# Kernel optimization log

Measured on AMD Instinct MI355X. Metric: run time of the kernel, lower is better.

## Reference

```python
import jax, jax.numpy as jnp
import numpy as np

N, E, B = 20000, 60000, 512
F_IN, ED, H, C = 7, 3, 4, 256
HC = H * C  # 1024
D_MODEL = 1024
EPS_BN = 1e-5


def setup_inputs() -> dict:
    key = jax.random.key(0)
    ks = jax.random.split(key, 24)
    s = 0.05
    inp = {
        'x': jax.random.normal(ks[0], (N, F_IN), jnp.float32),
        'edge_index': jax.random.randint(ks[1], (2, E), 0, N, jnp.int32),
        'edge_attr': jax.random.normal(ks[2], (E, ED), jnp.float32),
        'batch': jnp.sort(jax.random.randint(ks[3], (N,), 0, B, jnp.int32)),
        'w0': jax.random.normal(ks[4], (F_IN, HC), jnp.float32) * s,
        'w_rest': jax.random.normal(ks[5], (3, HC, HC), jnp.float32) * s,
        'w_edge': jax.random.normal(ks[6], (4, ED, HC), jnp.float32) * s,
        'att_src': jax.random.normal(ks[7], (4, H, C), jnp.float32) * s,
        'att_dst': jax.random.normal(ks[8], (4, H, C), jnp.float32) * s,
        'att_edge': jax.random.normal(ks[9], (4, H, C), jnp.float32) * s,
        'bias012': jax.random.normal(ks[10], (3, HC), jnp.float32) * s,
        'bias3': jax.random.normal(ks[11], (C,), jnp.float32) * s,
        'bn_gamma': jnp.ones((3, HC), jnp.float32),
        'bn_beta': jnp.zeros((3, HC), jnp.float32),
        'bn_mean': jnp.zeros((3, HC), jnp.float32),
        'bn_var': jnp.ones((3, HC), jnp.float32),
        'gate_w': jax.random.normal(ks[12], (C, 1), jnp.float32) * s,
        'gate_b': jnp.zeros((1,), jnp.float32),
        'proj_w': jax.random.normal(ks[13], (C, D_MODEL), jnp.float32) * s,
        'proj_b': jnp.zeros((D_MODEL,), jnp.float32),
    }
    return inp


def _gat_layer(x, ei, ea, W, We, a_s, a_d, a_e, bias, concat):
    # PyG GATConv with edge_dim, add_self_loops=True (fill_value='mean'), eval mode (no dropout)
    n = x.shape[0]
    sl = jnp.arange(n, dtype=ei.dtype)
    ea_mean = ea.mean(axis=0)
    ei = jnp.concatenate([ei, jnp.stack([sl, sl])], axis=1)            # [2, E+N]
    ea = jnp.concatenate([ea, jnp.broadcast_to(ea_mean, (n, ea.shape[1]))], axis=0)
    h = (x @ W).reshape(n, H, C)                                       # [N,H,C]
    alpha_src = jnp.einsum('nhc,hc->nh', h, a_s)
    alpha_dst = jnp.einsum('nhc,hc->nh', h, a_d)
    eh = (ea @ We).reshape(-1, H, C)
    alpha_e = jnp.einsum('ehc,hc->eh', eh, a_e)
    src, dst = ei[0], ei[1]
    alpha = jax.nn.leaky_relu(alpha_src[src] + alpha_dst[dst] + alpha_e, 0.2)  # [E+N,H]
    amax = jax.ops.segment_max(alpha, dst, num_segments=n)
    alpha = jnp.exp(alpha - amax[dst])
    denom = jax.ops.segment_sum(alpha, dst, num_segments=n)
    alpha = alpha / (denom[dst] + 1e-16)
    msg = h[src] * alpha[:, :, None]                                   # [E+N,H,C]
    out = jax.ops.segment_sum(msg, dst, num_segments=n)                # [N,H,C]
    out = out.reshape(n, H * C) if concat else out.mean(axis=1)
    return out + bias


def reference(x, edge_index, edge_attr, batch, w0, w_rest, w_edge, att_src, att_dst,
              att_edge, bias012, bias3, bn_gamma, bn_beta, bn_mean, bn_var,
              gate_w, gate_b, proj_w, proj_b):
    h = x
    for i in range(4):
        W = w0 if i == 0 else w_rest[i - 1]
        concat = i < 3
        b = bias012[i] if concat else bias3
        h = _gat_layer(h, edge_index, edge_attr, W, w_edge[i],
                       att_src[i], att_dst[i], att_edge[i], b, concat)
        if i < 3:
            # BatchNorm1d in eval mode, then ReLU (dropout is identity in eval)
            h = (h - bn_mean[i]) * (bn_gamma[i] / jnp.sqrt(bn_var[i] + EPS_BN)) + bn_beta[i]
            h = jax.nn.relu(h)
    # AttentionalAggregation: segment softmax over gate scores, weighted sum per graph
    gate = h @ gate_w + gate_b                                         # [N,1]
    gmax = jax.ops.segment_max(gate, batch, num_segments=B)
    g = jnp.exp(gate - gmax[batch])
    gsum = jax.ops.segment_sum(g, batch, num_segments=B)
    w = g / (gsum[batch] + 1e-16)
    graph = jax.ops.segment_sum(w * h, batch, num_segments=B)          # [B,256]
    return graph @ proj_w + proj_b                                     # [B,1024]
```

## Files before the change

### kernel.cpp

```cpp
#include <hip/hip_runtime.h>
#include <math.h>

#define NN 20000
#define NP 20480
#define EE 60000
#define BB 512
#define HC 1024
#define HH 4
#define CC 256

typedef _Float16 f16;
typedef f16 half8 __attribute__((ext_vector_type(8)));
typedef f16 f16x4 __attribute__((ext_vector_type(4)));
typedef float floatx4 __attribute__((ext_vector_type(4)));
typedef float floatx16 __attribute__((ext_vector_type(16)));

__device__ __forceinline__ size_t af_off(int n, int c) {
    int mblk = n >> 7, rr = n & 127;
    int iter = c >> 5, kc = c & 31;
    int kh = kc >> 4, kg = (kc >> 3) & 1, e = kc & 7;
    return ((((size_t)(mblk * 32 + iter) * 2 + kh) * 4 + (rr >> 5)) * 64 +
            (kg * 32 + (rr & 31))) * 8 + e;
}

__global__ void ea_sum_kernel(const float* __restrict__ ea, float* sums, int E_) {
    float s0 = 0.f, s1 = 0.f, s2 = 0.f;
    for (int e = blockIdx.x * 256 + threadIdx.x; e < E_; e += gridDim.x * 256) {
        s0 += ea[e * 3 + 0];
        s1 += ea[e * 3 + 1];
        s2 += ea[e * 3 + 2];
    }
    for (int o = 32; o; o >>= 1) {
        s0 += __shfl_down(s0, o);
        s1 += __shfl_down(s1, o);
        s2 += __shfl_down(s2, o);
    }
    if ((threadIdx.x & 63) == 0) {
        atomicAdd(&sums[0], s0);
        atomicAdd(&sums[1], s1);
        atomicAdd(&sums[2], s2);
    }
}

__global__ void hist_kernel(const int* __restrict__ ei, int* counts, int E_) {
    int e = blockIdx.x * 256 + threadIdx.x;
    if (e < E_) atomicAdd(&counts[ei[E_ + e]], 1);
}

__global__ void scan1_kernel(const int* __restrict__ counts, int* __restrict__ partial,
                             int* __restrict__ psums, int n) {
    __shared__ int sdata[256];
    int t = threadIdx.x;
    int i = blockIdx.x * 256 + t;
    int v = (i < n) ? counts[i] : 0;
    sdata[t] = v;
    __syncthreads();
#pragma unroll
    for (int off = 1; off < 256; off <<= 1) {
        int tmp = (t >= off) ? sdata[t - off] : 0;
        __syncthreads();
        sdata[t] += tmp;
        __syncthreads();
    }
    if (i < n) partial[i] = sdata[t];
    if (t == 255) psums[blockIdx.x] = sdata[255];
}

__global__ void scan2_kernel(int* __restrict__ psums, int nb) {
    __shared__ int sdata[128];
    int t = threadIdx.x;
    sdata[t] = (t < nb) ? psums[t] : 0;
    __syncthreads();
#pragma unroll
    for (int off = 1; off < 128; off <<= 1) {
        int tmp = (t >= off) ? sdata[t - off] : 0;
        __syncthreads();
        sdata[t] += tmp;
        __syncthreads();
    }
    if (t < nb) psums[t] = (t == 0) ? 0 : sdata[t - 1];
}

__global__ void scan3_kernel(const int* __restrict__ partial, const int* __restrict__ psums,
                             int* __restrict__ indptr, int n) {
    int i = blockIdx.x * 256 + threadIdx.x;
    if (i == 0) indptr[0] = 0;
    if (i < n) indptr[i + 1] = partial[i] + psums[blockIdx.x];
}

__global__ void scatter_kernel(const int* __restrict__ ei, const int* __restrict__ indptr,
                               int* fill, int* sorted, int* sdst, int E_) {
    int e = blockIdx.x * 256 + threadIdx.x;
    if (e >= E_) return;
    int d = ei[E_ + e];
    int pos = indptr[d] + atomicAdd(&fill[d], 1);
    sorted[pos] = e;
    sdst[pos] = d;
}

__global__ void bptr_kernel(const int* __restrict__ batch, int* bptr, int n, int nb) {
    int i = blockIdx.x * 256 + threadIdx.x;
    if (i >= n) return;
    int b = batch[i];
    if (i == 0) {
        for (int bb = 0; bb <= b; bb++) bptr[bb] = 0;
    } else {
        int pb = batch[i - 1];
        if (pb != b) {
            for (int bb = pb + 1; bb <= b; bb++) bptr[bb] = i;
        }
    }
    if (i == n - 1) {
        for (int bb = b + 1; bb <= nb; bb++) bptr[bb] = n;
    }
}

__global__ void wconv_kernel(const float* __restrict__ w_rest, f16* __restrict__ wt) {
    __shared__ float tile[64][65];
    int l = blockIdx.z;
    int bx = blockIdx.x * 64;
    int by = blockIdx.y * 64;
    int t = threadIdx.x;
    int tr = t >> 6, tc = t & 63;
#pragma unroll
    for (int i = 0; i < 16; i++) {
        int r = by + i * 4 + tr;
        tile[i * 4 + tr][tc] = w_rest[(size_t)l * 1048576 + (size_t)r * 1024 + bx + tc];
    }
    __syncthreads();
#pragma unroll
    for (int i = 0; i < 16; i++) {
        int n = bx + i * 4 + tr;
        wt[(size_t)l * 1048576 + (size_t)n * 1024 + by + tc] = (f16)tile[tc][i * 4 + tr];
    }
}

__global__ void bfrs_kernel(const f16* __restrict__ wt, f16* __restrict__ Bf) {
    int iter = blockIdx.x, nblk = blockIdx.y, l = blockIdx.z;
    const f16* wl = wt + (size_t)l * 1048576;
    f16* bl = Bf + (size_t)l * 1048576;
    int t = threadIdx.x;
    for (int c = t; c < 512; c += 256) {
        int kh = c >> 8, rem = c & 255, cg = rem >> 6, lane = rem & 63;
        int n = nblk * 128 + cg * 32 + (lane & 31);
        int k = iter * 32 + (kh * 2 + (lane >> 5)) * 8;
        half8 v = *(const half8*)&wl[(size_t)n * 1024 + k];
        *(half8*)&bl[(size_t)(nblk * 32 + iter) * 4096 + c * 8] = v;
    }
}

__global__ void mmat_all_kernel(const float* __restrict__ w_edge,
                                const float* __restrict__ att_edge,
                                const float* __restrict__ ea_sums, float* Mmat,
                                float* ae_self, float invE) {
    __shared__ float red[256];
    __shared__ float Ms[12];
    int l = blockIdx.x;
    int t = threadIdx.x;
    for (int dh = 0; dh < 12; dh++) {
        int d = dh >> 2, hh = dh & 3;
        float v = w_edge[l * 3072 + d * HC + hh * CC + t] * att_edge[l * HC + hh * CC + t];
        red[t] = v;
        __syncthreads();
        for (int o = 128; o; o >>= 1) {
            if (t < o) red[t] += red[t + o];
            __syncthreads();
        }
        if (t == 0) {
            Ms[dh] = red[0];
            Mmat[l * 12 + dh] = red[0];
        }
        __syncthreads();
    }
    if (t < 4) {
        float v = 0.f;
        for (int d = 0; d < 3; d++) v += ea_sums[d] * invE * Ms[d * 4 + t];
        ae_self[l * 4 + t] = v;
    }
}

__global__ void pack_kernel(const int* __restrict__ ei, const int* __restrict__ sorted,
                            const float* __restrict__ ea, const float* __restrict__ Mmat,
                            int* __restrict__ ssrc, float* __restrict__ aeh_pk) {
    int idx = blockIdx.x * 256 + threadIdx.x;
    if (idx >= EE) return;
    int eid = sorted[idx];
    ssrc[idx] = ei[eid];
    float a0 = ea[eid * 3 + 0], a1 = ea[eid * 3 + 1], a2 = ea[eid * 3 + 2];
#pragma unroll
    for (int l = 0; l < 4; l++) {
#pragma unroll
        for (int h = 0; h < 4; h++) {
            aeh_pk[(size_t)idx * 16 + l * 4 + h] =
                a0 * Mmat[l * 12 + h] + a1 * Mmat[l * 12 + 4 + h] + a2 * Mmat[l * 12 + 8 + h];
        }
    }
}

__global__ void edgep_kernel(const int* __restrict__ ssrc, const int* __restrict__ sdst,
                             const float* __restrict__ aeh_pk, const float* __restrict__ asrc,
                             const float* __restrict__ adst, float* __restrict__ pe,
                             int layer) {
    int i = blockIdx.x * 256 + threadIdx.x;
    if (i >= EE) return;
    int src = ssrc[i];
    int dst = sdst[i];
    float4 a = *(const float4*)&asrc[(size_t)src * 4];
    float4 d = *(const float4*)&adst[(size_t)dst * 4];
    float4 m = *(const float4*)&aeh_pk[(size_t)i * 16 + layer * 4];
    float r[4] = {a.x + d.x + m.x, a.y + d.y + m.y, a.z + d.z + m.z, a.w + d.w + m.w};
    float4 o;
#pragma unroll
    for (int k = 0; k < 4; k++) {
        float v = (r[k] > 0.f) ? r[k] : 0.2f * r[k];
        (&o.x)[k] = __expf(v);
    }
    *(float4*)&pe[(size_t)i * 4] = o;
}

__global__ void bnss_kernel(const float* __restrict__ bias012, const float* __restrict__ bn_g,
                            const float* __restrict__ bn_b, const float* __restrict__ bn_m,
                            const float* __restrict__ bn_v, float2* __restrict__ bnss) {
    int i = blockIdx.x * 256 + threadIdx.x;
    if (i >= 3 * HC) return;
    float s = bn_g[i] * rsqrtf(bn_v[i] + 1e-5f);
    float2 o;
    o.x = s;
    o.y = (bias012[i] - bn_m[i]) * s + bn_b[i];
    bnss[i] = o;
}

__global__ void wvec_kernel(const float* __restrict__ w_rest, const float* __restrict__ att_src,
                            const float* __restrict__ att_dst, float* __restrict__ wsv,
                            float* __restrict__ wdv) {
    int l = blockIdx.y;
    int k = blockIdx.x;
    int t = threadIdx.x;
    int hp = t >> 6, lane = t & 63;
    int col = hp * 256 + lane * 4;
    const float* wrow = w_rest + (size_t)l * 1048576 + (size_t)k * 1024;
    float4 w4 = *(const float4*)&wrow[col];
    float4 a4 = *(const float4*)&att_src[(l + 1) * HC + col];
    float4 d4 = *(const float4*)&att_dst[(l + 1) * HC + col];
    float sp = w4.x * a4.x + w4.y * a4.y + w4.z * a4.z + w4.w * a4.w;
    float dp = w4.x * d4.x + w4.y * d4.y + w4.z * d4.z + w4.w * d4.w;
    for (int m = 1; m < 64; m <<= 1) {
        sp += __shfl_xor(sp, m);
        dp += __shfl_xor(dp, m);
    }
    if (lane == 0) {
        wsv[((size_t)l * 1024 + k) * 4 + hp] = sp;
        wdv[((size_t)l * 1024 + k) * 4 + hp] = dp;
    }
}

__global__ void w0vec_kernel(const float* __restrict__ w0, const float* __restrict__ att_src,
                             const float* __restrict__ att_dst, float* __restrict__ w0s,
                             float* __restrict__ w0d) {
    int f = blockIdx.x;
    int t = threadIdx.x;
    int hp = t >> 6, lane = t & 63;
    int col = hp * 256 + lane * 4;
    float4 w4 = *(const float4*)&w0[f * HC + col];
    float4 a4 = *(const float4*)&att_src[col];
    float4 d4 = *(const float4*)&att_dst[col];
    float sp = w4.x * a4.x + w4.y * a4.y + w4.z * a4.z + w4.w * a4.w;
    float dp = w4.x * d4.x + w4.y * d4.y + w4.z * d4.z + w4.w * d4.w;
    for (int m = 1; m < 64; m <<= 1) {
        sp += __shfl_xor(sp, m);
        dp += __shfl_xor(dp, m);
    }
    if (lane == 0) {
        w0s[f * 4 + hp] = sp;
        w0d[f * 4 + hp] = dp;
    }
}

__global__ void alpha0_kernel(const float* __restrict__ x, const float* __restrict__ w0s,
                              const float* __restrict__ w0d, float* __restrict__ asrc,
                              float* __restrict__ adst) {
    int n = blockIdx.x * 256 + threadIdx.x;
    if (n >= NN) return;
    float xr[7];
#pragma unroll
    for (int f = 0; f < 7; f++) xr[f] = x[n * 7 + f];
#pragma unroll
    for (int hp = 0; hp < 4; hp++) {
        float s = 0.f, d = 0.f;
#pragma unroll
        for (int f = 0; f < 7; f++) {
            s += xr[f] * w0s[f * 4 + hp];
            d += xr[f] * w0d[f * 4 + hp];
        }
        asrc[n * 4 + hp] = s;
        adst[n * 4 + hp] = d;
    }
}

__global__ void agg0x_kernel(const float* __restrict__ x, const float* __restrict__ asrc,
                             const float* __restrict__ adst, const float* __restrict__ ae_self,
                             const int* __restrict__ ssrc, const float* __restrict__ pe,
                             const int* __restrict__ indptr, float* __restrict__ xagg) {
    int n = blockIdx.x * 256 + threadIdx.x;
    if (n >= NN) return;
    float4 as4 = *(const float4*)&asrc[(size_t)n * 4];
    float4 ad4 = *(const float4*)&adst[(size_t)n * 4];
    float adl[4] = {ad4.x, ad4.y, ad4.z, ad4.w};
    float asl[4] = {as4.x, as4.y, as4.z, as4.w};
    float xr[7];
#pragma unroll
    for (int f = 0; f < 7; f++) xr[f] = x[n * 7 + f];
    float denom[4];
    float xa[4][7];
#pragma unroll
    for (int h = 0; h < 4; h++) {
        float r = asl[h] + adl[h] + ae_self[h];
        r = (r > 0.f) ? r : 0.2f * r;
        float p = __expf(r);
        denom[h] = p;
#pragma unroll
        for (int f = 0; f < 7; f++) xa[h][f] = p * xr[f];
    }
    int s = indptr[n], e = indptr[n + 1];
    for (int idx = s; idx < e; idx++) {
        int src = ssrc[idx];
        float4 pv = *(const float4*)&pe[(size_t)idx * 4];
        float pl[4] = {pv.x, pv.y, pv.z, pv.w};
        float xs[7];
#pragma unroll
        for (int f = 0; f < 7; f++) xs[f] = x[src * 7 + f];
#pragma unroll
        for (int h = 0; h < 4; h++) {
            denom[h] += pl[h];
#pragma unroll
            for (int f = 0; f < 7; f++) xa[h][f] += pl[h] * xs[f];
        }
    }
#pragma unroll
    for (int h = 0; h < 4; h++) {
        float inv = 1.0f / (denom[h] + 1e-16f);
#pragma unroll
        for (int f = 0; f < 7; f++) xagg[(size_t)n * 28 + h * 7 + f] = xa[h][f] * inv;
    }
}

__global__ void gemm7f_kernel(const float* __restrict__ xagg, const float* __restrict__ w0,
                              const float2* __restrict__ bnss, const float* __restrict__ wsv,
                              const float* __restrict__ wdv, f16* __restrict__ outAf,
                              float* __restrict__ asrc_n, float* __restrict__ adst_n) {
    __shared__ float xs[28];
    __shared__ float red[32];
    int n = blockIdx.x, t = threadIdx.x;
    if (t < 28) xs[t] = xagg[(size_t)n * 28 + t];
    __syncthreads();
    int head = t >> 6;
    int j0 = t * 4;
    float sp[4] = {0.f, 0.f, 0.f, 0.f}, dp[4] = {0.f, 0.f, 0.f, 0.f};
    f16x4 o;
#pragma unroll
    for (int k = 0; k < 4; k++) {
        int j = j0 + k;
        float dot = 0.f;
#pragma unroll
        for (int f = 0; f < 7; f++) dot += xs[head * 7 + f] * w0[f * HC + j];
        float2 ss = bnss[j];
        float val = fmaxf(fmaf(dot, ss.x, ss.y), 0.f);
        o[k] = (f16)val;
        float4 w4s = *(const float4*)&wsv[(size_t)j * 4];
        float4 w4d = *(const float4*)&wdv[(size_t)j * 4];
        sp[0] += val * w4s.x; sp[1] += val * w4s.y;
        sp[2] += val * w4s.z; sp[3] += val * w4s.w;
        dp[0] += val * w4d.x; dp[1] += val * w4d.y;
        dp[2] += val * w4d.z; dp[3] += val * w4d.w;
    }
    *(f16x4*)&outAf[af_off(n, j0)] = o;
    int wave = t >> 6, lane = t & 63;
#pragma unroll
    for (int m = 1; m < 64; m <<= 1) {
#pragma unroll
        for (int j = 0; j < 4; j++) {
            sp[j] += __shfl_xor(sp[j], m);
            dp[j] += __shfl_xor(dp[j], m);
        }
    }
    if (lane == 0) {
#pragma unroll
        for (int j = 0; j < 4; j++) {
            red[wave * 8 + j] = sp[j];
            red[wave * 8 + 4 + j] = dp[j];
        }
    }
    __syncthreads();
    if (t < 8) {
        float v = red[t] + red[8 + t] + red[16 + t] + red[24 + t];
        if (t < 4) asrc_n[n * 4 + t] = v;
        else adst_n[n * 4 + (t - 4)] = v;
    }
}

__global__ __launch_bounds__(256) void mfma_gemm_kernel(const f16* __restrict__ Af,
                                                        const f16* __restrict__ Bf,
                                                        f16* __restrict__ C16) {
    int t = threadIdx.x;
    int wave = t >> 6, lane = t & 63;
    int gid = blockIdx.x;
    int g = gid >> 6, rblk = gid & 63;
    int nblk = rblk >> 3;
    int mblk = g * 8 + (rblk & 7);
    int rg0 = (wave >> 1) * 2;
    int cg0 = (wave & 1) * 2;

    floatx16 acc[2][2];
#pragma unroll
    for (int i = 0; i < 2; i++)
#pragma unroll
        for (int j = 0; j < 2; j++) acc[i][j] = (floatx16)(0.f);

    const f16* pa = Af + (size_t)mblk * 131072 + (size_t)lane * 8;
    const f16* pb = Bf + (size_t)nblk * 131072 + (size_t)lane * 8;

#pragma unroll 2
    for (int iter = 0; iter < 32; iter++) {
        size_t base = (size_t)iter * 4096;
        half8 afr[2][2], bfr[2][2];
#pragma unroll
        for (int kh = 0; kh < 2; kh++) {
#pragma unroll
            for (int i = 0; i < 2; i++) {
                afr[kh][i] = *(const half8*)&pa[base + kh * 2048 + (rg0 + i) * 512];
                bfr[kh][i] = *(const half8*)&pb[base + kh * 2048 + (cg0 + i) * 512];
            }
        }
#pragma unroll
        for (int kh = 0; kh < 2; kh++)
#pragma unroll
            for (int i = 0; i < 2; i++)
#pragma unroll
                for (int j = 0; j < 2; j++)
                    acc[i][j] = __builtin_amdgcn_mfma_f32_32x32x16_f16(bfr[kh][j], afr[kh][i],
                                                                       acc[i][j], 0, 0, 0);
    }

    int fr32 = lane & 31, kg = lane >> 5;
#pragma unroll
    for (int i = 0; i < 2; i++) {
        int row = mblk * 128 + rg0 * 32 + i * 32 + fr32;
#pragma unroll
        for (int j = 0; j < 2; j++) {
#pragma unroll
            for (int gq = 0; gq < 4; gq++) {
                f16x4 o;
#pragma unroll
                for (int r = 0; r < 4; r++) o[r] = (f16)acc[i][j][gq * 4 + r];
                *(f16x4*)&C16[(size_t)row * HC + nblk * 128 + cg0 * 32 + j * 32 + gq * 8 +
                              kg * 4] = o;
            }
        }
    }
}

__global__ void agg_kernel(const f16* __restrict__ h16, const float* __restrict__ asrc,
                           const float* __restrict__ adst, const float* __restrict__ ae_self,
                           const int* __restrict__ ssrc, const float* __restrict__ pe,
                           const int* __restrict__ indptr, const float2* __restrict__ bnss,
                           const float* __restrict__ wsv, const float* __restrict__ wdv,
                           const float* __restrict__ bias3, const float* __restrict__ gw,
                           const float* __restrict__ gb, f16* __restrict__ out16,
                           float* __restrict__ asrc_n, float* __restrict__ adst_n,
                           float* __restrict__ out3, float* __restrict__ gate,
                           int layer, int concat) {
    __shared__ float buf[1024];
    __shared__ float red[32];
    int n = blockIdx.x, t = threadIdx.x;
    int h = t >> 6, lane = t & 63;
    int c4 = t * 4;

    float r = asrc[n * 4 + h] + adst[n * 4 + h] + ae_self[layer * 4 + h];
    r = (r > 0.f) ? r : 0.2f * r;
    float p = __expf(r);
    float denom = p;
    float ax, ay, az, aw;
    {
        f16x4 v = *(const f16x4*)&h16[(size_t)n * HC + c4];
        ax = p * (float)v[0]; ay = p * (float)v[1];
        az = p * (float)v[2]; aw = p * (float)v[3];
    }
    int s = indptr[n], epos = indptr[n + 1];
    for (int base = s; base < epos; base += 4) {
        int rem = epos - base;
        int src[4];
        float pv[4];
#pragma unroll
        for (int j = 0; j < 4; j++) {
            if (j < rem) {
                src[j] = ssrc[base + j];
                pv[j] = pe[(size_t)(base + j) * 4 + h];
            } else {
                src[j] = n;
                pv[j] = 0.f;
            }
        }
        f16x4 u[4];
#pragma unroll
        for (int j = 0; j < 4; j++) u[j] = *(const f16x4*)&h16[(size_t)src[j] * HC + c4];
#pragma unroll
        for (int j = 0; j < 4; j++) {
            denom += pv[j];
            ax += pv[j] * (float)u[j][0];
            ay += pv[j] * (float)u[j][1];
            az += pv[j] * (float)u[j][2];
            aw += pv[j] * (float)u[j][3];
        }
    }
    float inv = 1.0f / (denom + 1e-16f);
    ax *= inv; ay *= inv; az *= inv; aw *= inv;

    if (concat) {
        float vals[4] = {ax, ay, az, aw};
        f16x4 o;
        float sp[4] = {0.f, 0.f, 0.f, 0.f}, dp[4] = {0.f, 0.f, 0.f, 0.f};
#pragma unroll
        for (int k = 0; k < 4; k++) {
            int j = c4 + k;
            float2 ss = bnss[j];
            float val = fmaxf(fmaf(vals[k], ss.x, ss.y), 0.f);
            o[k] = (f16)val;
            float4 w4s = *(const float4*)&wsv[(size_t)j * 4];
            float4 w4d = *(const float4*)&wdv[(size_t)j * 4];
            sp[0] += val * w4s.x; sp[1] += val * w4s.y;
            sp[2] += val * w4s.z; sp[3] += val * w4s.w;
            dp[0] += val * w4d.x; dp[1] += val * w4d.y;
            dp[2] += val * w4d.z; dp[3] += val * w4d.w;
        }
        *(f16x4*)&out16[af_off(n, c4)] = o;
#pragma unroll
        for (int m = 1; m < 64; m <<= 1) {
#pragma unroll
            for (int j = 0; j < 4; j++) {
                sp[j] += __shfl_xor(sp[j], m);
                dp[j] += __shfl_xor(dp[j], m);
            }
        }
        if (lane == 0) {
#pragma unroll
            for (int j = 0; j < 4; j++) {
                red[h * 8 + j] = sp[j];
                red[h * 8 + 4 + j] = dp[j];
            }
        }
        __syncthreads();
        if (t < 8) {
            float v = red[t] + red[8 + t] + red[16 + t] + red[24 + t];
            if (t < 4) asrc_n[n * 4 + t] = v;
            else adst_n[n * 4 + (t - 4)] = v;
        }
    } else {
        buf[c4 + 0] = ax;
        buf[c4 + 1] = ay;
        buf[c4 + 2] = az;
        buf[c4 + 3] = aw;
        __syncthreads();
        if (t < 64) {
            float gpart = 0.f;
#pragma unroll
            for (int k = 0; k < 4; k++) {
                int c = t * 4 + k;
                float v2 = 0.25f * (buf[c] + buf[256 + c] + buf[512 + c] + buf[768 + c]) +
                           bias3[c];
                out3[(size_t)n * CC + c] = v2;
                gpart += v2 * gw[c];
            }
            for (int o = 32; o; o >>= 1) gpart += __shfl_down(gpart, o);
            if (t == 0) gate[n] = gpart + gb[0];
        }
    }
}

__global__ void graphagg_kernel(const float* __restrict__ gate, const float* __restrict__ h3,
                                const int* __restrict__ bptr, float* __restrict__ graph) {
    __shared__ float red[256];
    __shared__ float wn[256];
    int b = blockIdx.x, t = threadIdx.x;
    int s = bptr[b], epos = bptr[b + 1];
    float m = -3.4e38f;
    for (int n = s + t; n < epos; n += 256) m = fmaxf(m, gate[n]);
    red[t] = m;
    __syncthreads();
    for (int o = 128; o; o >>= 1) {
        if (t < o) red[t] = fmaxf(red[t], red[t + o]);
        __syncthreads();
    }
    float mval = red[0];
    __syncthreads();
    float sum = 0.f;
    for (int n = s + t; n < epos; n += 256) sum += __expf(gate[n] - mval);
    red[t] = sum;
    __syncthreads();
    for (int o = 128; o; o >>= 1) {
        if (t < o) red[t] += red[t + o];
        __syncthreads();
    }
    float ssum = red[0];
    __syncthreads();
    float acc = 0.f;
    for (int base = s; base < epos; base += 256) {
        int n = base + t;
        wn[t] = (n < epos) ? __expf(gate[n] - mval) : 0.f;
        __syncthreads();
        int cnt = min(256, epos - base);
        for (int j = 0; j < cnt; j++) acc += wn[j] * h3[(size_t)(base + j) * CC + t];
        __syncthreads();
    }
    graph[b * CC + t] = acc / (ssum + 1e-16f);
}

__global__ void proj_kernel(const float* __restrict__ graph, const float* __restrict__ pw,
                            const float* __restrict__ pb, float* __restrict__ out) {
    __shared__ float g[256];
    int b = blockIdx.x, t = threadIdx.x;
    g[t] = graph[b * CC + t];
    __syncthreads();
    for (int j = t; j < 1024; j += 256) {
        float acc = pb[j];
        for (int c = 0; c < 256; c++) acc += g[c] * pw[c * 1024 + j];
        out[(size_t)b * 1024 + j] = acc;
    }
}

extern "C" void kernel_launch(void* const* d_in, const int* in_sizes, int n_in,
                              void* d_out, int out_size, void* d_ws, size_t ws_size,
                              hipStream_t stream) {
    const float* x = (const float*)d_in[0];
    const int* ei = (const int*)d_in[1];
    const float* ea = (const float*)d_in[2];
    const int* batch = (const int*)d_in[3];
    const float* w0 = (const float*)d_in[4];
    const float* w_rest = (const float*)d_in[5];
    const float* w_edge = (const float*)d_in[6];
    const float* att_src = (const float*)d_in[7];
    const float* att_dst = (const float*)d_in[8];
    const float* att_edge = (const float*)d_in[9];
    const float* bias012 = (const float*)d_in[10];
    const float* bias3 = (const float*)d_in[11];
    const float* bn_g = (const float*)d_in[12];
    const float* bn_b = (const float*)d_in[13];
    const float* bn_m = (const float*)d_in[14];
    const float* bn_v = (const float*)d_in[15];
    const float* gate_w = (const float*)d_in[16];
    const float* gate_b = (const float*)d_in[17];
    const float* proj_w = (const float*)d_in[18];
    const float* proj_b = (const float*)d_in[19];
    float* out = (float*)d_out;

    float* ws = (float*)d_ws;
    size_t off = 0;
    f16* h_lin = (f16*)(ws + off); off += (size_t)NP * HC / 2;
    f16* h_af = (f16*)(ws + off); off += (size_t)NP * HC / 2;
    float* h3 = ws + off; off += (size_t)NN * CC;
    f16* wt = (f16*)(ws + off); off += (size_t)3 * HC * HC / 2;
    f16* Bf = (f16*)(ws + off); off += (size_t)3 * HC * HC / 2;
    float* asrcA = ws + off; off += (size_t)NN * 4;
    float* adstA = ws + off; off += (size_t)NN * 4;
    float* asrcB = ws + off; off += (size_t)NN * 4;
    float* adstB = ws + off; off += (size_t)NN * 4;
    float* wsv = ws + off; off += (size_t)3 * HC * 4;
    float* wdv = ws + off; off += (size_t)3 * HC * 4;
    float* w0s = ws + off; off += 28;
    float* w0d = ws + off; off += 28;
    float2* bnss = (float2*)(ws + off); off += (size_t)3 * HC * 2;
    float* aeh_pk = ws + off; off += (size_t)EE * 16;
    float* pbuf = ws + off; off += (size_t)EE * 4;
    float* xagg = ws + off; off += (size_t)NN * 28;
    float* gate = ws + off; off += (size_t)NN;
    float* graph = ws + off; off += (size_t)BB * CC;
    float* ea_sums = ws + off; off += 4;
    float* Mmat = ws + off; off += 48;
    float* ae_self = ws + off; off += 16;
    int* counts = (int*)(ws + off); off += NN;
    int* partial = (int*)(ws + off); off += NN;
    int* psums = (int*)(ws + off); off += 128;
    int* indptr = (int*)(ws + off); off += NN + 1;
    int* fill = (int*)(ws + off); off += NN;
    int* sorted = (int*)(ws + off); off += EE;
    int* ssrc = (int*)(ws + off); off += EE;
    int* sdst = (int*)(ws + off); off += EE;
    int* bptr = (int*)(ws + off); off += BB + 1;

    hipMemsetAsync(ea_sums, 0, 4 * sizeof(float), stream);
    hipMemsetAsync(counts, 0, NN * sizeof(int), stream);
    hipMemsetAsync(fill, 0, NN * sizeof(int), stream);

    ea_sum_kernel<<<64, 256, 0, stream>>>(ea, ea_sums, EE);
    hist_kernel<<<(EE + 255) / 256, 256, 0, stream>>>(ei, counts, EE);
    int nblk = (NN + 255) / 256;
    scan1_kernel<<<nblk, 256, 0, stream>>>(counts, partial, psums, NN);
    scan2_kernel<<<1, 128, 0, stream>>>(psums, nblk);
    scan3_kernel<<<nblk, 256, 0, stream>>>(partial, psums, indptr, NN);
    scatter_kernel<<<(EE + 255) / 256, 256, 0, stream>>>(ei, indptr, fill, sorted, sdst, EE);
    bptr_kernel<<<(NN + 255) / 256, 256, 0, stream>>>(batch, bptr, NN, BB);
    wconv_kernel<<<dim3(16, 16, 3), 256, 0, stream>>>(w_rest, wt);
    bfrs_kernel<<<dim3(32, 8, 3), 256, 0, stream>>>(wt, Bf);
    mmat_all_kernel<<<4, 256, 0, stream>>>(w_edge, att_edge, ea_sums, Mmat, ae_self,
                                           1.0f / EE);
    pack_kernel<<<(EE + 255) / 256, 256, 0, stream>>>(ei, sorted, ea, Mmat, ssrc, aeh_pk);
    bnss_kernel<<<(3 * HC + 255) / 256, 256, 0, stream>>>(bias012, bn_g, bn_b, bn_m, bn_v,
                                                          bnss);
    wvec_kernel<<<dim3(1024, 3), 256, 0, stream>>>(w_rest, att_src, att_dst, wsv, wdv);
    w0vec_kernel<<<7, 256, 0, stream>>>(w0, att_src, att_dst, w0s, w0d);
    alpha0_kernel<<<(NN + 255) / 256, 256, 0, stream>>>(x, w0s, w0d, asrcA, adstA);

    edgep_kernel<<<(EE + 255) / 256, 256, 0, stream>>>(ssrc, sdst, aeh_pk, asrcA, adstA,
                                                       pbuf, 0);
    agg0x_kernel<<<(NN + 255) / 256, 256, 0, stream>>>(x, asrcA, adstA, ae_self, ssrc,
                                                       pbuf, indptr, xagg);
    gemm7f_kernel<<<NN, 256, 0, stream>>>(xagg, w0, bnss, wsv, wdv, h_af, asrcB, adstB);

    float* asrc_cur = asrcB;
    float* adst_cur = adstB;
    float* asrc_nxt = asrcA;
    float* adst_nxt = adstA;
    for (int i = 1; i < 4; i++) {
        mfma_gemm_kernel<<<(NP / 128) * (HC / 128), 256, 0, stream>>>(
            h_af, Bf + (size_t)(i - 1) * HC * HC, h_lin);
        edgep_kernel<<<(EE + 255) / 256, 256, 0, stream>>>(ssrc, sdst, aeh_pk, asrc_cur,
                                                           adst_cur, pbuf, i);
        agg_kernel<<<NN, 256, 0, stream>>>(
            h_lin, asrc_cur, adst_cur, ae_self, ssrc, pbuf, indptr, bnss + (size_t)i * HC,
            wsv + (size_t)i * HC * 4, wdv + (size_t)i * HC * 4, bias3, gate_w, gate_b,
            h_af, asrc_nxt, adst_nxt, h3, gate, i, (i < 3) ? 1 : 0);
        float* tmp = asrc_cur; asrc_cur = asrc_nxt; asrc_nxt = tmp;
        tmp = adst_cur; adst_cur = adst_nxt; adst_nxt = tmp;
    }

    graphagg_kernel<<<BB, 256, 0, stream>>>(gate, h3, bptr, graph);
    proj_kernel<<<BB, 256, 0, stream>>>(graph, proj_w, proj_b, out);
}
```

Before: 680.6 us.

## Map one node per wavefront in aggregation and layer-0 GEMM kernels

The agg and gemm7f kernels move from one 256-thread block per node to one 64-lane wavefront per node, with each lane handling 16 contiguous channels through 16-byte half8 loads. Cross-head reductions now use wave shuffles instead of shared memory and __syncthreads, and the final-layer head averaging uses xor shuffles across the 16-lane groups. This removes block-level synchronization and shared-memory traffic and widens the neighbor gather loads. In exchange it uses more registers per lane and has fewer waves in flight per node, which may lower occupancy and the memory parallelism available to the gathers.

```diff
diff --git a/kernel.cpp b/kernel.cpp
--- a/kernel.cpp
+++ b/kernel.cpp
@@ -348,24 +348,41 @@
                               const float2* __restrict__ bnss, const float* __restrict__ wsv,
                               const float* __restrict__ wdv, f16* __restrict__ outAf,
                               float* __restrict__ asrc_n, float* __restrict__ adst_n) {
-    __shared__ float xs[28];
-    __shared__ float red[32];
-    int n = blockIdx.x, t = threadIdx.x;
-    if (t < 28) xs[t] = xagg[(size_t)n * 28 + t];
-    __syncthreads();
-    int head = t >> 6;
-    int j0 = t * 4;
+    int t = threadIdx.x;
+    int wv = t >> 6, lane = t & 63;
+    int n = blockIdx.x * 4 + wv;
+    int h = lane >> 4;
+    int cb = lane << 4;
+
+    float xv = (lane < 28) ? xagg[(size_t)n * 28 + lane] : 0.f;
+    float xs[7];
+#pragma unroll
+    for (int f = 0; f < 7; f++) xs[f] = __shfl(xv, h * 7 + f);
+
+    float dot[16];
+#pragma unroll
+    for (int k = 0; k < 16; k++) dot[k] = 0.f;
+#pragma unroll
+    for (int f = 0; f < 7; f++) {
+        const float* wrow = w0 + (size_t)f * HC + cb;
+#pragma unroll
+        for (int k = 0; k < 16; k += 4) {
+            float4 w4 = *(const float4*)&wrow[k];
+            dot[k + 0] += xs[f] * w4.x;
+            dot[k + 1] += xs[f] * w4.y;
+            dot[k + 2] += xs[f] * w4.z;
+            dot[k + 3] += xs[f] * w4.w;
+        }
+    }
+
     float sp[4] = {0.f, 0.f, 0.f, 0.f}, dp[4] = {0.f, 0.f, 0.f, 0.f};
-    f16x4 o;
-#pragma unroll
-    for (int k = 0; k < 4; k++) {
-        int j = j0 + k;
-        float dot = 0.f;
-#pragma unroll
-        for (int f = 0; f < 7; f++) dot += xs[head * 7 + f] * w0[f * HC + j];
+    half8 o0, o1;
+#pragma unroll
+    for (int k = 0; k < 8; k++) {
+        int j = cb + k;
         float2 ss = bnss[j];
-        float val = fmaxf(fmaf(dot, ss.x, ss.y), 0.f);
-        o[k] = (f16)val;
+        float val = fmaxf(fmaf(dot[k], ss.x, ss.y), 0.f);
+        o0[k] = (f16)val;
         float4 w4s = *(const float4*)&wsv[(size_t)j * 4];
         float4 w4d = *(const float4*)&wdv[(size_t)j * 4];
         sp[0] += val * w4s.x; sp[1] += val * w4s.y;
@@ -373,8 +390,21 @@
         dp[0] += val * w4d.x; dp[1] += val * w4d.y;
         dp[2] += val * w4d.z; dp[3] += val * w4d.w;
     }
-    *(f16x4*)&outAf[af_off(n, j0)] = o;
-    int wave = t >> 6, lane = t & 63;
+#pragma unroll
+    for (int k = 0; k < 8; k++) {
+        int j = cb + 8 + k;
+        float2 ss = bnss[j];
+        float val = fmaxf(fmaf(dot[8 + k], ss.x, ss.y), 0.f);
+        o1[k] = (f16)val;
+        float4 w4s = *(const float4*)&wsv[(size_t)j * 4];
+        float4 w4d = *(const float4*)&wdv[(size_t)j * 4];
+        sp[0] += val * w4s.x; sp[1] += val * w4s.y;
+        sp[2] += val * w4s.z; sp[3] += val * w4s.w;
+        dp[0] += val * w4d.x; dp[1] += val * w4d.y;
+        dp[2] += val * w4d.z; dp[3] += val * w4d.w;
+    }
+    *(half8*)&outAf[af_off(n, cb)] = o0;
+    *(half8*)&outAf[af_off(n, cb + 8)] = o1;
 #pragma unroll
     for (int m = 1; m < 64; m <<= 1) {
 #pragma unroll
@@ -384,17 +414,11 @@
         }
     }
     if (lane == 0) {
-#pragma unroll
-        for (int j = 0; j < 4; j++) {
-            red[wave * 8 + j] = sp[j];
-            red[wave * 8 + 4 + j] = dp[j];
-        }
-    }
-    __syncthreads();
-    if (t < 8) {
-        float v = red[t] + red[8 + t] + red[16 + t] + red[24 + t];
-        if (t < 4) asrc_n[n * 4 + t] = v;
-        else adst_n[n * 4 + (t - 4)] = v;
+        float4 so, ddo;
+        so.x = sp[0]; so.y = sp[1]; so.z = sp[2]; so.w = sp[3];
+        ddo.x = dp[0]; ddo.y = dp[1]; ddo.z = dp[2]; ddo.w = dp[3];
+        *(float4*)&asrc_n[(size_t)n * 4] = so;
+        *(float4*)&adst_n[(size_t)n * 4] = ddo;
     }
 }
 
@@ -469,21 +493,25 @@
                            float* __restrict__ asrc_n, float* __restrict__ adst_n,
                            float* __restrict__ out3, float* __restrict__ gate,
                            int layer, int concat) {
-    __shared__ float buf[1024];
-    __shared__ float red[32];
-    int n = blockIdx.x, t = threadIdx.x;
-    int h = t >> 6, lane = t & 63;
-    int c4 = t * 4;
+    int t = threadIdx.x;
+    int wv = t >> 6, lane = t & 63;
+    int n = blockIdx.x * 4 + wv;
+    int h = lane >> 4;
+    int cb = lane << 4;
 
     float r = asrc[n * 4 + h] + adst[n * 4 + h] + ae_self[layer * 4 + h];
     r = (r > 0.f) ? r : 0.2f * r;
     float p = __expf(r);
     float denom = p;
-    float ax, ay, az, aw;
+    float acc[16];
     {
-        f16x4 v = *(const f16x4*)&h16[(size_t)n * HC + c4];
-        ax = p * (float)v[0]; ay = p * (float)v[1];
-        az = p * (float)v[2]; aw = p * (float)v[3];
+        half8 v0 = *(const half8*)&h16[(size_t)n * HC + cb];
+        half8 v1 = *(const half8*)&h16[(size_t)n * HC + cb + 8];
+#pragma unroll
+        for (int k = 0; k < 8; k++) {
+            acc[k] = p * (float)v0[k];
+            acc[8 + k] = p * (float)v1[k];
+        }
     }
     int s = indptr[n], epos = indptr[n + 1];
     for (int base = s; base < epos; base += 4) {
@@ -500,31 +528,35 @@
                 pv[j] = 0.f;
             }
         }
-        f16x4 u[4];
-#pragma unroll
-        for (int j = 0; j < 4; j++) u[j] = *(const f16x4*)&h16[(size_t)src[j] * HC + c4];
+        half8 u0[4], u1[4];
+#pragma unroll
+        for (int j = 0; j < 4; j++) {
+            u0[j] = *(const half8*)&h16[(size_t)src[j] * HC + cb];
+            u1[j] = *(const half8*)&h16[(size_t)src[j] * HC + cb + 8];
+        }
 #pragma unroll
         for (int j = 0; j < 4; j++) {
             denom += pv[j];
-            ax += pv[j] * (float)u[j][0];
-            ay += pv[j] * (float)u[j][1];
-            az += pv[j] * (float)u[j][2];
-            aw += pv[j] * (float)u[j][3];
+#pragma unroll
+            for (int k = 0; k < 8; k++) {
+                acc[k] += pv[j] * (float)u0[j][k];
+                acc[8 + k] += pv[j] * (float)u1[j][k];
+            }
         }
     }
     float inv = 1.0f / (denom + 1e-16f);
-    ax *= inv; ay *= inv; az *= inv; aw *= inv;
+#pragma unroll
+    for (int k = 0; k < 16; k++) acc[k] *= inv;
 
     if (concat) {
-        float vals[4] = {ax, ay, az, aw};
-        f16x4 o;
         float sp[4] = {0.f, 0.f, 0.f, 0.f}, dp[4] = {0.f, 0.f, 0.f, 0.f};
-#pragma unroll
-        for (int k = 0; k < 4; k++) {
-            int j = c4 + k;
+        half8 o0, o1;
+#pragma unroll
+        for (int k = 0; k < 8; k++) {
+            int j = cb + k;
             float2 ss = bnss[j];
-            float val = fmaxf(fmaf(vals[k], ss.x, ss.y), 0.f);
-            o[k] = (f16)val;
+            float val = fmaxf(fmaf(acc[k], ss.x, ss.y), 0.f);
+            o0[k] = (f16)val;
             float4 w4s = *(const float4*)&wsv[(size_t)j * 4];
             float4 w4d = *(const float4*)&wdv[(size_t)j * 4];
             sp[0] += val * w4s.x; sp[1] += val * w4s.y;
@@ -532,7 +564,21 @@
             dp[0] += val * w4d.x; dp[1] += val * w4d.y;
             dp[2] += val * w4d.z; dp[3] += val * w4d.w;
         }
-        *(f16x4*)&out16[af_off(n, c4)] = o;
+#pragma unroll
+        for (int k = 0; k < 8; k++) {
+            int j = cb + 8 + k;
+            float2 ss = bnss[j];
+            float val = fmaxf(fmaf(acc[8 + k], ss.x, ss.y), 0.f);
+            o1[k] = (f16)val;
+            float4 w4s = *(const float4*)&wsv[(size_t)j * 4];
+            float4 w4d = *(const float4*)&wdv[(size_t)j * 4];
+            sp[0] += val * w4s.x; sp[1] += val * w4s.y;
+            sp[2] += val * w4s.z; sp[3] += val * w4s.w;
+            dp[0] += val * w4d.x; dp[1] += val * w4d.y;
+            dp[2] += val * w4d.z; dp[3] += val * w4d.w;
+        }
+        *(half8*)&out16[af_off(n, cb)] = o0;
+        *(half8*)&out16[af_off(n, cb + 8)] = o1;
 #pragma unroll
         for (int m = 1; m < 64; m <<= 1) {
 #pragma unroll
@@ -542,37 +588,37 @@
             }
         }
         if (lane == 0) {
-#pragma unroll
-            for (int j = 0; j < 4; j++) {
-                red[h * 8 + j] = sp[j];
-                red[h * 8 + 4 + j] = dp[j];
+            float4 so, ddo;
+            so.x = sp[0]; so.y = sp[1]; so.z = sp[2]; so.w = sp[3];
+            ddo.x = dp[0]; ddo.y = dp[1]; ddo.z = dp[2]; ddo.w = dp[3];
+            *(float4*)&asrc_n[(size_t)n * 4] = so;
+            *(float4*)&adst_n[(size_t)n * 4] = ddo;
+        }
+    } else {
+#pragma unroll
+        for (int k = 0; k < 16; k++) {
+            acc[k] += __shfl_xor(acc[k], 16);
+            acc[k] += __shfl_xor(acc[k], 32);
+        }
+        int cw = (lane & 15) << 4;
+        float gpart = 0.f;
+        float v2[16];
+#pragma unroll
+        for (int k = 0; k < 16; k++) {
+            v2[k] = 0.25f * acc[k] + bias3[cw + k];
+            gpart += v2[k] * gw[cw + k];
+        }
+        if (lane < 16) {
+#pragma unroll
+            for (int k = 0; k < 16; k += 4) {
+                float4 o;
+                o.x = v2[k]; o.y = v2[k + 1]; o.z = v2[k + 2]; o.w = v2[k + 3];
+                *(float4*)&out3[(size_t)n * CC + cw + k] = o;
             }
         }
-        __syncthreads();
-        if (t < 8) {
-            float v = red[t] + red[8 + t] + red[16 + t] + red[24 + t];
-            if (t < 4) asrc_n[n * 4 + t] = v;
-            else adst_n[n * 4 + (t - 4)] = v;
-        }
-    } else {
-        buf[c4 + 0] = ax;
-        buf[c4 + 1] = ay;
-        buf[c4 + 2] = az;
-        buf[c4 + 3] = aw;
-        __syncthreads();
-        if (t < 64) {
-            float gpart = 0.f;
-#pragma unroll
-            for (int k = 0; k < 4; k++) {
-                int c = t * 4 + k;
-                float v2 = 0.25f * (buf[c] + buf[256 + c] + buf[512 + c] + buf[768 + c]) +
-                           bias3[c];
-                out3[(size_t)n * CC + c] = v2;
-                gpart += v2 * gw[c];
-            }
-            for (int o = 32; o; o >>= 1) gpart += __shfl_down(gpart, o);
-            if (t == 0) gate[n] = gpart + gb[0];
-        }
+#pragma unroll
+        for (int m = 1; m < 16; m <<= 1) gpart += __shfl_xor(gpart, m);
+        if (lane == 0) gate[n] = gpart + gb[0];
     }
 }
 
@@ -713,7 +759,7 @@
                                                        pbuf, 0);
     agg0x_kernel<<<(NN + 255) / 256, 256, 0, stream>>>(x, asrcA, adstA, ae_self, ssrc,
                                                        pbuf, indptr, xagg);
-    gemm7f_kernel<<<NN, 256, 0, stream>>>(xagg, w0, bnss, wsv, wdv, h_af, asrcB, adstB);
+    gemm7f_kernel<<<NN / 4, 256, 0, stream>>>(xagg, w0, bnss, wsv, wdv, h_af, asrcB, adstB);
 
     float* asrc_cur = asrcB;
     float* adst_cur = adstB;
@@ -724,7 +770,7 @@
             h_af, Bf + (size_t)(i - 1) * HC * HC, h_lin);
         edgep_kernel<<<(EE + 255) / 256, 256, 0, stream>>>(ssrc, sdst, aeh_pk, asrc_cur,
                                                            adst_cur, pbuf, i);
-        agg_kernel<<<NN, 256, 0, stream>>>(
+        agg_kernel<<<NN / 4, 256, 0, stream>>>(
             h_lin, asrc_cur, adst_cur, ae_self, ssrc, pbuf, indptr, bnss + (size_t)i * HC,
             wsv + (size_t)i * HC * 4, wdv + (size_t)i * HC * 4, bias3, gate_w, gate_b,
             h_af, asrc_nxt, adst_nxt, h3, gate, i, (i < 3) ? 1 : 0);
```

After: 898.5 us. 1.32x slower.
